# Performance work log

Measured on AMD Instinct MI355X. Metric: run time of the kernel, lower is better.

## Reference

```python
import jax, jax.numpy as jnp
import numpy as np

Q_N = 65536   # queries
KV_N = 65536  # keys/values
C = 256       # channels
H = 8         # heads
D = C // H
N_E = 524288  # edges
SCALE = 1.0 / np.sqrt(C).astype(np.float32)  # sim_scale/sqrt(num_ch), sim_scale=1
LN_EPS = 1e-5


def setup_inputs() -> dict:
    key = jax.random.key(0)
    ks = jax.random.split(key, 8)
    q = jax.random.normal(ks[0], (Q_N, C), jnp.float32)
    k = jax.random.normal(ks[1], (KV_N, C), jnp.float32)
    bias = jax.random.normal(ks[2], (N_E, H), jnp.float32) * 0.1
    src = jax.random.randint(ks[3], (N_E,), 0, KV_N)
    dst = jnp.sort(jax.random.randint(ks[4], (N_E,), 0, Q_N))
    wq = jax.random.normal(ks[5], (C, C), jnp.float32) * 0.02
    wk = jax.random.normal(ks[6], (C, C), jnp.float32) * 0.02
    wo = jax.random.normal(ks[7], (C, C), jnp.float32) * 0.02
    return {
        "q": q, "k": k, "bias": bias,
        "ln_w": jnp.ones((C,), jnp.float32), "ln_b": jnp.zeros((C,), jnp.float32),
        "wq": wq, "bq": jnp.zeros((C,), jnp.float32),
        "wk": wk, "bk": jnp.zeros((C,), jnp.float32),
        "wo": wo, "bo": jnp.zeros((C,), jnp.float32),
        "src": src, "dst": dst,
    }


def _layernorm(x, w, b):
    mu = jnp.mean(x, axis=-1, keepdims=True)
    var = jnp.var(x, axis=-1, keepdims=True)
    return (x - mu) * jax.lax.rsqrt(var + LN_EPS) * w + b


def reference(q, k, bias, ln_w, ln_b, wq, bq, wk, bk, wo, bo, src, dst):
    residual = q
    qn = _layernorm(q, ln_w, ln_b)           # norm_loc='pre'
    qp = qn @ wq.T + bq                       # [Q, C]
    kp = k @ wk.T + bk                        # [KV, C]; same_kv -> v = kp
    # gather per-edge, split heads: [N, H, D]
    qe = qp[dst].reshape(N_E, H, D)
    ke = kp[src].reshape(N_E, H, D)
    sim = (jnp.sum(qe * ke, axis=-1) + bias) * SCALE   # [N, H]
    # segment-max per dst (init -inf, matching index_reduce amax)
    max_sim = jax.ops.segment_max(sim, dst, num_segments=Q_N)  # [Q, H]
    e = jnp.exp(sim - max_sim[dst])
    wsum = 1e-8 + jax.ops.segment_sum(e, dst, num_segments=Q_N)  # [Q, H]
    weights = e / wsum[dst]                   # [N, H]
    out_e = (ke * weights[..., None]).reshape(N_E, C)  # weighted values (v=k)
    out = jax.ops.segment_sum(out_e, dst, num_segments=Q_N)  # [Q, C]
    out = out @ wo.T + bo + residual
    return out, weights
```

## Files before the change

kernel.cpp:

```cpp
#include <hip/hip_runtime.h>
#include <cmath>

#define QN    65536
#define KVN   65536
#define CD    256
#define NH    8
#define NE    524288
#define SCL   0.0625f
#define LNEPS 1e-5f
#define LOG2E 1.4426950408889634f

typedef __bf16 bf16x8 __attribute__((ext_vector_type(8)));
typedef float  f32x4  __attribute__((ext_vector_type(4)));

__device__ __forceinline__ float b2f(ushort u) {
    return __builtin_bit_cast(float, (unsigned)u << 16);
}
__device__ __forceinline__ float blo(unsigned u) {
    return __builtin_bit_cast(float, u << 16);
}
__device__ __forceinline__ float bhi(unsigned u) {
    return __builtin_bit_cast(float, u & 0xFFFF0000u);
}
__device__ __forceinline__ ushort f2bf(float f) {
    unsigned u = __builtin_bit_cast(unsigned, f);
    return (ushort)((u + 0x7FFFu + ((u >> 16) & 1u)) >> 16);
}

#if __has_builtin(__builtin_amdgcn_exp2f)
__device__ __forceinline__ float fexp2(float x) { return __builtin_amdgcn_exp2f(x); }
#else
__device__ __forceinline__ float fexp2(float x) {
    float r; asm volatile("v_exp_f32 %0, %1" : "=v"(r) : "v"(x)); return r;
}
#endif

#define GLD16(g, l) __builtin_amdgcn_global_load_lds( \
    (const __attribute__((address_space(1))) unsigned int*)(const void*)(g), \
    (__attribute__((address_space(3))) unsigned int*)(void*)(l), 16, 0, 0)

#define LNB   (QN / 4)
#define RLB   (NE / 256)
__global__ __launch_bounds__(256) void prep_k(const float* __restrict__ q,
                                              const float* __restrict__ k,
                                              const float* __restrict__ lnw,
                                              const float* __restrict__ lnb,
                                              const float* __restrict__ wq,
                                              const float* __restrict__ wk,
                                              const float* __restrict__ wo,
                                              const int* __restrict__ dst,
                                              ushort* __restrict__ qn,
                                              ushort* __restrict__ kb,
                                              ushort* __restrict__ wb,
                                              int* __restrict__ row_lo) {
    const int blk = blockIdx.x;
    if (blk < LNB) {
        int row  = (blk << 2) + (threadIdx.x >> 6);
        int lane = threadIdx.x & 63;
        float4 v = *(const float4*)(q + (size_t)row * CD + (lane << 2));
        float s  = v.x + v.y + v.z + v.w;
        float s2 = v.x * v.x + v.y * v.y + v.z * v.z + v.w * v.w;
        #pragma unroll
        for (int m = 1; m < 64; m <<= 1) {
            s  += __shfl_xor(s, m);
            s2 += __shfl_xor(s2, m);
        }
        float mu   = s * (1.0f / CD);
        float rstd = rsqrtf(s2 * (1.0f / CD) - mu * mu + LNEPS);
        float4 w = *(const float4*)(lnw + (lane << 2));
        float4 b = *(const float4*)(lnb + (lane << 2));
        ushort4 o;
        o.x = f2bf((v.x - mu) * rstd * w.x + b.x);
        o.y = f2bf((v.y - mu) * rstd * w.y + b.y);
        o.z = f2bf((v.z - mu) * rstd * w.z + b.z);
        o.w = f2bf((v.w - mu) * rstd * w.w + b.w);
        *(ushort4*)(qn + (size_t)row * CD + (lane << 2)) = o;
    } else if (blk < LNB + 192) {
        int idx4 = ((blk - LNB) * 256 + threadIdx.x) * 4;
        int mat  = idx4 >> 16;
        int off  = idx4 & 65535;
        const float* src = (mat == 0) ? wq : (mat == 1) ? wk : wo;
        float4 v = *(const float4*)(src + off);
        ushort4 o;
        o.x = f2bf(v.x); o.y = f2bf(v.y); o.z = f2bf(v.z); o.w = f2bf(v.w);
        *(ushort4*)(wb + idx4) = o;
    } else if (blk < LNB + 192 + RLB) {
        int e = (blk - LNB - 192) * 256 + threadIdx.x;
        int d     = dst[e];
        int dprev = (e == 0) ? -1 : dst[e - 1];
        for (int qq = dprev + 1; qq <= d; ++qq) row_lo[qq] = e;
        if (e == NE - 1)
            for (int qq = d + 1; qq <= QN; ++qq) row_lo[qq] = NE;
    } else {
        int row  = ((blk - LNB - 192 - RLB) << 2) + (threadIdx.x >> 6);
        int lane = threadIdx.x & 63;
        float4 v = *(const float4*)(k + (size_t)row * CD + (lane << 2));
        ushort4 o;
        o.x = f2bf(v.x); o.y = f2bf(v.y); o.z = f2bf(v.z); o.w = f2bf(v.w);
        *(ushort4*)(kb + (size_t)row * CD + (lane << 2)) = o;
    }
}

template<int EPI, int NT>
__global__ __launch_bounds__(512) void gemm2_k(const ushort* __restrict__ A0,
                                               const ushort* __restrict__ A1,
                                               const ushort* __restrict__ B0,
                                               const ushort* __restrict__ B1,
                                               const float* __restrict__ bias0,
                                               const float* __restrict__ bias1,
                                               const float* __restrict__ resid,
                                               void* __restrict__ C0,
                                               void* __restrict__ C1) {
    const bool second = (blockIdx.z != 0);
    const ushort* Ap   = second ? A1 : A0;
    const ushort* B    = second ? B1 : B0;
    const float*  bias = second ? bias1 : bias0;
    void*         Cout = second ? C1 : C0;

    __shared__ __align__(16) ushort Bs[8][4096];
    __shared__ __align__(16) ushort As[8][4096];

    const int t    = threadIdx.x;
    const int lane = t & 63;
    const int wid  = t >> 6;
    const int wm   = wid & 1;
    const int wn   = wid >> 1;
    const size_t bn  = (size_t)blockIdx.y * 128;
    size_t bm = (size_t)blockIdx.x * (NT * 128);

    const int sr = t >> 2;
    const int sc = (t & 3) * 8;

    constexpr int E = (EPI == 0) ? 8 : 16;

    f32x4 acc[4][2] = {};
    f32x4 biasv[2];
    #pragma unroll
    for (int ni = 0; ni < 2; ++ni)
        biasv[ni] = *(const f32x4*)(bias + bn + wn * 32 + ni * 16 + ((lane >> 4) << 2));

    #pragma unroll
    for (int s = 0; s < 8; ++s)
        GLD16(B + (bn + sr) * CD + (s << 5) + sc, &Bs[s][wid << 9]);
    #pragma unroll
    for (int s = 0; s < 6; ++s)
        GLD16(Ap + (bm + sr) * CD + (s << 5) + sc, &As[s][wid << 9]);
    asm volatile("" : "+v"(biasv[0]), "+v"(biasv[1]));

#define KSTEP(KT, VM, GUARD)                                                          \
  {                                                                                   \
    if (GUARD) {                                                                      \
      const ushort* ga_ = Ap + (bm + (((KT) >= 2) ? 128 : 0) + sr) * CD               \
                          + ((((KT) + 6) & 7) << 5) + sc;                             \
      GLD16(ga_, &As[((KT) + 6) & 7][wid << 9]);                                      \
    }                                                                                 \
    asm volatile("s_waitcnt vmcnt(%0) lgkmcnt(0)\n\ts_barrier" :: "i"(VM) : "memory");\
    {                                                                                 \
      const int kq_ = (lane >> 4) << 3;                                               \
      bf16x8 af_[4], bg_[2];                                                          \
      _Pragma("unroll")                                                               \
      for (int mi = 0; mi < 4; ++mi)                                                  \
        af_[mi] = *(const bf16x8*)&As[(KT) & 7][((wm * 64 + mi * 16 + (lane & 15)) << 5) + kq_]; \
      _Pragma("unroll")                                                               \
      for (int ni = 0; ni < 2; ++ni)                                                  \
        bg_[ni] = *(const bf16x8*)&Bs[(KT)][((wn * 32 + ni * 16 + (lane & 15)) << 5) + kq_];     \
      _Pragma("unroll")                                                               \
      for (int mi = 0; mi < 4; ++mi)                                                  \
        _Pragma("unroll")                                                             \
        for (int ni = 0; ni < 2; ++ni)                                                \
          acc[mi][ni] = __builtin_amdgcn_mfma_f32_16x16x32_bf16(bg_[ni], af_[mi], acc[mi][ni], 0, 0, 0); \
    }                                                                                 \
  }

#define EPILOG()                                                                      \
  {                                                                                   \
    _Pragma("unroll")                                                                 \
    for (int mi = 0; mi < 4; ++mi) {                                                  \
      const size_t row_ = bm + wm * 64 + mi * 16 + (lane & 15);                       \
      _Pragma("unroll")                                                               \
      for (int ni = 0; ni < 2; ++ni) {                                                \
        const size_t col_ = bn + wn * 32 + ni * 16 + ((lane >> 4) << 2);              \
        if (EPI == 0) {                                                               \
          ushort4 o_;                                                                 \
          o_.x = f2bf(acc[mi][ni][0] + biasv[ni][0]);                                 \
          o_.y = f2bf(acc[mi][ni][1] + biasv[ni][1]);                                 \
          o_.z = f2bf(acc[mi][ni][2] + biasv[ni][2]);                                 \
          o_.w = f2bf(acc[mi][ni][3] + biasv[ni][3]);                                 \
          *(ushort4*)((ushort*)Cout + row_ * CD + col_) = o_;                         \
        } else {                                                                      \
          f32x4 rs_ = *(const f32x4*)(resid + row_ * CD + col_);                      \
          f32x4 o_;                                                                   \
          o_[0] = acc[mi][ni][0] + biasv[ni][0] + rs_[0];                             \
          o_[1] = acc[mi][ni][1] + biasv[ni][1] + rs_[1];                             \
          o_[2] = acc[mi][ni][2] + biasv[ni][2] + rs_[2];                             \
          o_[3] = acc[mi][ni][3] + biasv[ni][3] + rs_[3];                             \
          *(f32x4*)((float*)Cout + row_ * CD + col_) = o_;                            \
        }                                                                             \
        acc[mi][ni] = (f32x4){0.f, 0.f, 0.f, 0.f};                                    \
      }                                                                               \
    }                                                                                 \
    asm volatile("" ::: "memory");                                                    \
  }

    KSTEP(0, 6, 1) KSTEP(1, 6, 1) KSTEP(2, 6, 1) KSTEP(3, 6, 1)
    KSTEP(4, 6, 1) KSTEP(5, 6, 1) KSTEP(6, 6, 1) KSTEP(7, 6, 1)
    EPILOG();
    bm += 128;

    for (int tt = 1; tt < NT - 1; ++tt) {
        KSTEP(0, 6 + E, 1) KSTEP(1, 6 + E, 1) KSTEP(2, 6 + E, 1) KSTEP(3, 6 + E, 1)
        KSTEP(4, 6 + E, 1) KSTEP(5, 6 + E, 1) KSTEP(6, 6, 1)     KSTEP(7, 6, 1)
        EPILOG();
        bm += 128;
    }

    KSTEP(0, 6 + E, 1) KSTEP(1, 6 + E, 1) KSTEP(2, 5 + E, 0) KSTEP(3, 4 + E, 0)
    KSTEP(4, 3 + E, 0) KSTEP(5, 2 + E, 0) KSTEP(6, 1, 0)     KSTEP(7, 0, 0)
    EPILOG();

#undef KSTEP
#undef EPILOG
}

__global__ __launch_bounds__(64) void edge_attn_k(const ushort* __restrict__ qp,
                                                  const ushort* __restrict__ kp,
                                                  const float* __restrict__ bias,
                                                  const int* __restrict__ src,
                                                  const int* __restrict__ row_lo,
                                                  ushort* __restrict__ ao,
                                                  float* __restrict__ simw) {
    const int q    = blockIdx.x;
    const int lane = threadIdx.x;
    const int e    = lane >> 3;
    const int h    = lane & 7;
    const int lo = row_lo[q];
    const int hi = row_lo[q + 1];
    const int deg = hi - lo;
    const float SC2 = SCL * LOG2E;

    __shared__ __align__(16) float red[64 * 36];

    uint4 qr[4];
    {
        const uint4* qrp = (const uint4*)(qp + (size_t)q * CD + (h << 5));
        qr[0] = qrp[0]; qr[1] = qrp[1]; qr[2] = qrp[2]; qr[3] = qrp[3];
    }

    f32x4 acc4[8] = {};
    float m = -INFINITY, s = 0.f;
    float wval0 = -INFINITY, wval1 = -INFINITY;

    for (int base = lo; base < hi; base += 8) {
        const bool act = (base + e) < hi;
        int   sv = 0;
        float bv = 0.f;
        if (act) {
            sv = src[base + e];
            bv = bias[(size_t)base * NH + lane] * SC2;
        }
        uint4 ku[4] = {};
        if (act) {
            const uint4* kr = (const uint4*)(kp + (size_t)sv * CD + (h << 5));
            ku[0] = kr[0]; ku[1] = kr[1]; ku[2] = kr[2]; ku[3] = kr[3];
        }
        float d = 0.f;
        #pragma unroll
        for (int j = 0; j < 4; ++j) {
            const unsigned qu[4] = {qr[j].x, qr[j].y, qr[j].z, qr[j].w};
            const unsigned kw[4] = {ku[j].x, ku[j].y, ku[j].z, ku[j].w};
            #pragma unroll
            for (int w = 0; w < 4; ++w) {
                d = fmaf(blo(qu[w]), blo(kw[w]), d);
                d = fmaf(bhi(qu[w]), bhi(kw[w]), d);
            }
        }
        float sim = act ? fmaf(d, SC2, bv) : -INFINITY;

        float cmax = sim;
        cmax = fmaxf(cmax, __shfl_xor(cmax, 8));
        cmax = fmaxf(cmax, __shfl_xor(cmax, 16));
        cmax = fmaxf(cmax, __shfl_xor(cmax, 32));
        const float mnew  = fmaxf(m, cmax);
        const float scale = fexp2(m - mnew);
        const float ex    = fexp2(sim - mnew);
        s = s * scale + ex;
        #pragma unroll
        for (int jj = 0; jj < 8; ++jj) {
            acc4[jj][0] *= scale; acc4[jj][1] *= scale;
            acc4[jj][2] *= scale; acc4[jj][3] *= scale;
        }
        #pragma unroll
        for (int j = 0; j < 4; ++j) {
            const unsigned kw[4] = {ku[j].x, ku[j].y, ku[j].z, ku[j].w};
            #pragma unroll
            for (int w = 0; w < 4; ++w) {
                const int qd = j * 2 + (w >> 1);
                const int el = (w & 1) * 2;
                acc4[qd][el]     = fmaf(ex, blo(kw[w]), acc4[qd][el]);
                acc4[qd][el + 1] = fmaf(ex, bhi(kw[w]), acc4[qd][el + 1]);
            }
        }
        m = mnew;

        if (deg <= 16) {
            if (base == lo) wval0 = sim; else wval1 = sim;
        } else if (act) {
            simw[(size_t)base * NH + lane] = sim;
        }
    }

    s += __shfl_xor(s, 8);
    s += __shfl_xor(s, 16);
    s += __shfl_xor(s, 32);
    const float inv = 1.0f / (s + 1e-8f);

    #pragma unroll
    for (int jj = 0; jj < 8; ++jj)
        *(f32x4*)&red[lane * 36 + jj * 4] = acc4[jj];
    __syncthreads();
    f32x4 sum = {};
    #pragma unroll
    for (int ep = 0; ep < 8; ++ep) {
        const f32x4 p = *(const f32x4*)&red[((ep << 3) + h) * 36 + (e << 2)];
        sum[0] += p[0]; sum[1] += p[1]; sum[2] += p[2]; sum[3] += p[3];
    }
    ushort4 o;
    o.x = f2bf(sum[0] * inv);
    o.y = f2bf(sum[1] * inv);
    o.z = f2bf(sum[2] * inv);
    o.w = f2bf(sum[3] * inv);
    *(ushort4*)(ao + (size_t)q * CD + (h << 5) + (e << 2)) = o;

    if (deg > 0) {
        if (deg <= 8) {
            if (lane < (deg << 3))
                simw[(size_t)lo * NH + lane] = fexp2(wval0 - m) * inv;
        } else if (deg <= 16) {
            simw[(size_t)lo * NH + lane] = fexp2(wval0 - m) * inv;
            if (lane < ((deg - 8) << 3))
                simw[(size_t)(lo + 8) * NH + lane] = fexp2(wval1 - m) * inv;
        } else {
            asm volatile("s_waitcnt vmcnt(0)" ::: "memory");
            for (int i = lane; i < deg * 8; i += 64) {
                size_t idx = (size_t)lo * NH + i;
                float v = simw[idx];
                simw[idx] = fexp2(v - m) * inv;
            }
        }
    }
}

extern "C" void kernel_launch(void* const* d_in, const int* in_sizes, int n_in,
                              void* d_out, int out_size, void* d_ws, size_t ws_size,
                              hipStream_t stream) {
    const float* q    = (const float*)d_in[0];
    const float* k    = (const float*)d_in[1];
    const float* bias = (const float*)d_in[2];
    const float* lnw  = (const float*)d_in[3];
    const float* lnb  = (const float*)d_in[4];
    const float* wq   = (const float*)d_in[5];
    const float* bq   = (const float*)d_in[6];
    const float* wk   = (const float*)d_in[7];
    const float* bk   = (const float*)d_in[8];
    const float* wo   = (const float*)d_in[9];
    const float* bo   = (const float*)d_in[10];
    const int*   src  = (const int*)d_in[11];
    const int*   dst  = (const int*)d_in[12];

    float* out_m = (float*)d_out;
    float* out_w = out_m + (size_t)QN * CD;

    ushort* qn_b = (ushort*)d_ws;
    ushort* qp_b = qn_b + (size_t)QN * CD;
    ushort* kp_b = qp_b + (size_t)QN * CD;
    ushort* wb   = kp_b + (size_t)KVN * CD;
    int*    rowlo = (int*)(wb + 3 * 65536);

    ushort* kb = (ushort*)d_out;

    prep_k<<<dim3(LNB + 192 + RLB + LNB), dim3(256), 0, stream>>>(
        q, k, lnw, lnb, wq, wk, wo, dst, qn_b, kb, wb, rowlo);

    gemm2_k<0, 8><<<dim3(64, 2, 2), dim3(512), 0, stream>>>(
        qn_b, kb, wb, wb + 65536, bq, bk, nullptr, qp_b, kp_b);

    edge_attn_k<<<dim3(QN), dim3(64), 0, stream>>>(
        qp_b, kp_b, bias, src, rowlo, qn_b , out_w);

    gemm2_k<1, 4><<<dim3(128, 2, 1), dim3(512), 0, stream>>>(
        qn_b, qn_b, wb + 131072, wb + 131072, bo, bo, q, out_m, out_m);
}
```

Before: 175.9 us.

## Repartition edge attention so each lane owns a channel slice across all edges

Changes the thread mapping in the edge attention kernel. Previously each lane handled one edge-head pair with a full 32-channel row and reduced accumulators through shared memory. Now each lane owns 4 channels of one head and walks all 8 edges of a chunk, computing partial dots that are reduced with cross-lane shuffles. This removes the shared-memory reduction, the barrier and most register pressure (one f32x4 accumulator instead of eight). In exchange it adds many shuffles per chunk and issues narrower 8-byte gathers per lane.

```diff
diff --git a/kernel.cpp b/kernel.cpp
--- a/kernel.cpp
+++ b/kernel.cpp
@@ -238,97 +238,89 @@
     const int deg = hi - lo;
     const float SC2 = SCL * LOG2E;
 
-    __shared__ __align__(16) float red[64 * 36];
-
-    uint4 qr[4];
-    {
-        const uint4* qrp = (const uint4*)(qp + (size_t)q * CD + (h << 5));
-        qr[0] = qrp[0]; qr[1] = qrp[1]; qr[2] = qrp[2]; qr[3] = qrp[3];
-    }
-
-    f32x4 acc4[8] = {};
+    const uint2 qv2 = *(const uint2*)(qp + (size_t)q * CD + (h << 5) + (e << 2));
+
+    f32x4 acc = {0.f, 0.f, 0.f, 0.f};
     float m = -INFINITY, s = 0.f;
     float wval0 = -INFINITY, wval1 = -INFINITY;
 
     for (int base = lo; base < hi; base += 8) {
-        const bool act = (base + e) < hi;
-        int   sv = 0;
+        int sv = 0;
+        if (lane < 8 && base + lane < hi) sv = src[base + lane];
         float bv = 0.f;
-        if (act) {
-            sv = src[base + e];
-            bv = bias[(size_t)base * NH + lane] * SC2;
-        }
-        uint4 ku[4] = {};
-        if (act) {
-            const uint4* kr = (const uint4*)(kp + (size_t)sv * CD + (h << 5));
-            ku[0] = kr[0]; ku[1] = kr[1]; ku[2] = kr[2]; ku[3] = kr[3];
-        }
-        float d = 0.f;
-        #pragma unroll
-        for (int j = 0; j < 4; ++j) {
-            const unsigned qu[4] = {qr[j].x, qr[j].y, qr[j].z, qr[j].w};
-            const unsigned kw[4] = {ku[j].x, ku[j].y, ku[j].z, ku[j].w};
+        if (lane < (hi - base) * 8) bv = bias[(size_t)base * NH + lane] * SC2;
+
+        uint2 ku[8];
+        #pragma unroll
+        for (int ep = 0; ep < 8; ++ep) {
+            ku[ep].x = 0u; ku[ep].y = 0u;
+            if (base + ep < hi) {
+                int sidx = __shfl(sv, ep);
+                ku[ep] = *(const uint2*)(kp + (size_t)sidx * CD + (h << 5) + (e << 2));
+            }
+        }
+        float p[8];
+        #pragma unroll
+        for (int ep = 0; ep < 8; ++ep) {
+            float d;
+            d = blo(qv2.x) * blo(ku[ep].x);
+            d = fmaf(bhi(qv2.x), bhi(ku[ep].x), d);
+            d = fmaf(blo(qv2.y), blo(ku[ep].y), d);
+            d = fmaf(bhi(qv2.y), bhi(ku[ep].y), d);
+            p[ep] = d;
+        }
+        #pragma unroll
+        for (int r = 8; r <= 32; r <<= 1) {
             #pragma unroll
-            for (int w = 0; w < 4; ++w) {
-                d = fmaf(blo(qu[w]), blo(kw[w]), d);
-                d = fmaf(bhi(qu[w]), bhi(kw[w]), d);
-            }
-        }
-        float sim = act ? fmaf(d, SC2, bv) : -INFINITY;
-
-        float cmax = sim;
-        cmax = fmaxf(cmax, __shfl_xor(cmax, 8));
-        cmax = fmaxf(cmax, __shfl_xor(cmax, 16));
-        cmax = fmaxf(cmax, __shfl_xor(cmax, 32));
+            for (int ep = 0; ep < 8; ++ep)
+                p[ep] += __shfl_xor(p[ep], r);
+        }
+        float sims[8];
+        #pragma unroll
+        for (int ep = 0; ep < 8; ++ep) {
+            float bvp = __shfl(bv, (ep << 3) + h);
+            sims[ep] = (base + ep < hi) ? fmaf(p[ep], SC2, bvp) : -INFINITY;
+        }
+        float cmax = sims[0];
+        #pragma unroll
+        for (int ep = 1; ep < 8; ++ep) cmax = fmaxf(cmax, sims[ep]);
         const float mnew  = fmaxf(m, cmax);
         const float scale = fexp2(m - mnew);
-        const float ex    = fexp2(sim - mnew);
-        s = s * scale + ex;
-        #pragma unroll
-        for (int jj = 0; jj < 8; ++jj) {
-            acc4[jj][0] *= scale; acc4[jj][1] *= scale;
-            acc4[jj][2] *= scale; acc4[jj][3] *= scale;
-        }
-        #pragma unroll
-        for (int j = 0; j < 4; ++j) {
-            const unsigned kw[4] = {ku[j].x, ku[j].y, ku[j].z, ku[j].w};
-            #pragma unroll
-            for (int w = 0; w < 4; ++w) {
-                const int qd = j * 2 + (w >> 1);
-                const int el = (w & 1) * 2;
-                acc4[qd][el]     = fmaf(ex, blo(kw[w]), acc4[qd][el]);
-                acc4[qd][el + 1] = fmaf(ex, bhi(kw[w]), acc4[qd][el + 1]);
-            }
-        }
+        acc[0] *= scale; acc[1] *= scale; acc[2] *= scale; acc[3] *= scale;
+        float esum = 0.f;
+        #pragma unroll
+        for (int ep = 0; ep < 8; ++ep) {
+            const float ex = fexp2(sims[ep] - mnew);
+            esum += ex;
+            acc[0] = fmaf(ex, blo(ku[ep].x), acc[0]);
+            acc[1] = fmaf(ex, bhi(ku[ep].x), acc[1]);
+            acc[2] = fmaf(ex, blo(ku[ep].y), acc[2]);
+            acc[3] = fmaf(ex, bhi(ku[ep].y), acc[3]);
+        }
+        s = s * scale + esum;
         m = mnew;
 
+        float ta = (e & 1) ? sims[1] : sims[0];
+        float tb = (e & 1) ? sims[3] : sims[2];
+        float tc = (e & 1) ? sims[5] : sims[4];
+        float td = (e & 1) ? sims[7] : sims[6];
+        float te = (e & 2) ? tb : ta;
+        float tf = (e & 2) ? td : tc;
+        float own = (e & 4) ? tf : te;
         if (deg <= 16) {
-            if (base == lo) wval0 = sim; else wval1 = sim;
-        } else if (act) {
-            simw[(size_t)base * NH + lane] = sim;
+            if (base == lo) wval0 = own; else wval1 = own;
+        } else if (base + e < hi) {
+            simw[(size_t)base * NH + lane] = own;
         }
     }
 
-    s += __shfl_xor(s, 8);
-    s += __shfl_xor(s, 16);
-    s += __shfl_xor(s, 32);
     const float inv = 1.0f / (s + 1e-8f);
 
-    #pragma unroll
-    for (int jj = 0; jj < 8; ++jj)
-        *(f32x4*)&red[lane * 36 + jj * 4] = acc4[jj];
-    __syncthreads();
-    f32x4 sum = {};
-    #pragma unroll
-    for (int ep = 0; ep < 8; ++ep) {
-        const f32x4 p = *(const f32x4*)&red[((ep << 3) + h) * 36 + (e << 2)];
-        sum[0] += p[0]; sum[1] += p[1]; sum[2] += p[2]; sum[3] += p[3];
-    }
     ushort4 o;
-    o.x = f2bf(sum[0] * inv);
-    o.y = f2bf(sum[1] * inv);
-    o.z = f2bf(sum[2] * inv);
-    o.w = f2bf(sum[3] * inv);
+    o.x = f2bf(acc[0] * inv);
+    o.y = f2bf(acc[1] * inv);
+    o.z = f2bf(acc[2] * inv);
+    o.w = f2bf(acc[3] * inv);
     *(ushort4*)(ao + (size_t)q * CD + (h << 5) + (e << 2)) = o;
 
     if (deg > 0) {
```

After: 175.4 us. No clear change (-0.3%).
